# Kernel optimization log

Hardware: AMD Instinct MI355X
Metric: run time of the kernel (lower is better)

Reference implementation:

```python
import jax, jax.numpy as jnp
import numpy as np
import math

LOG_2PI = math.log(2.0 * math.pi)
ETA = 1.0        # Beta(gamma_1=1, gamma_2=eta) stick-breaking prior (gamma buffers at init)
MC_NUM = 4096    # Monte-Carlo samples
T_CLUSTER = 2    # trunc (must be 2: original normalize_factor broadcast requires it)
T_CLS = 2        # classifier DP truncation
DIM = 1024
N = 65536


def mix_weights(b):
    # stick-breaking: pad(b,(0,1),1) * pad(cumprod(1-b),(1,0),1); b: [..., T] -> [..., T+1]
    b1m = jnp.cumprod(1.0 - b, axis=-1)
    ones = jnp.ones((*b.shape[:-1], 1), b.dtype)
    return jnp.concatenate([b, ones], axis=-1) * jnp.concatenate([ones, b1m], axis=-1)


def gauss_log_prob(x, mu, rho):
    # diag Gaussian log-prob summed over feature dim; x [N,D], mu/rho [T,D] -> [N,T]
    std = jnp.log1p(jnp.exp(rho))                      # sigma = log(1+exp(rho))
    inv_var = 1.0 / (std * std)
    const = -0.5 * x.shape[-1] * LOG_2PI - jnp.sum(jnp.log(std), axis=-1)  # [T]
    # 0.5*sum((x-mu)^2/var) expanded as matmuls to avoid an [N,T,D] intermediate
    quad = 0.5 * ((x * x) @ inv_var.T) - x @ (mu * inv_var).T \
           + 0.5 * jnp.sum(mu * mu * inv_var, axis=-1)
    return const - quad


def gauss_entropy(rho):
    # mean over T of diag-Gaussian entropies; rho [T,D] -> scalar
    D = rho.shape[-1]
    std = jnp.log1p(jnp.exp(rho))
    ent = 0.5 * D * (LOG_2PI + 1.0) + jnp.sum(jnp.log(std), axis=-1)  # [T]
    return jnp.mean(ent)


def setup_inputs() -> dict:
    key = jax.random.key(0)
    ks = jax.random.split(key, 5)
    return {
        "x": jax.random.normal(ks[0], (N, DIM), jnp.float32),
        "mu_c": jax.random.normal(ks[1], (T_CLUSTER, DIM), jnp.float32),
        "rho_c": jax.random.normal(ks[2], (T_CLUSTER, DIM), jnp.float32),
        "mu_f": jax.random.normal(ks[3], (T_CLS, DIM), jnp.float32),
        "rho_f": jax.random.normal(ks[4], (T_CLS, DIM), jnp.float32),
    }


def reference(x, mu_c, rho_c, mu_f, rho_f):
    key = jax.random.key(1)
    k1, k2, k3, k4, k5 = jax.random.split(key, 5)

    # ---- D_P_cluster.likelihood(x) ----
    beta_lik = jax.random.beta(k1, 1.0, ETA, (x.shape[0], T_CLUSTER), x.dtype)
    pi_lik = mix_weights(beta_lik)[:, :-1]                 # [N, T]
    ent = gauss_entropy(rho_c)                             # scalar
    log_pdfs = gauss_log_prob(x, mu_c, rho_c)              # [N, T]
    phi = jax.nn.softmax(jnp.log(pi_lik) + ent + log_pdfs, axis=-1)
    neg_likelihood = -jnp.mean(jnp.sum(phi * (ent + log_pdfs), axis=1))

    # ---- MC sampling from the cluster mixture (fused, no Python loop) ----
    betas = jax.random.beta(k2, 1.0, ETA, (MC_NUM, T_CLUSTER), x.dtype)
    w = mix_weights(betas)[:, :-1]                         # [MC, T]
    w = w / jnp.sum(w, axis=1, keepdims=True)              # row-normalize (T==2 makes this exact)
    draws = jax.random.categorical(k3, jnp.log(w), axis=-1)  # [MC] component indices
    eps = jax.random.normal(k4, (MC_NUM, DIM), x.dtype)
    std_c = jnp.log1p(jnp.exp(rho_c))
    mc_samples = mu_c[draws] + std_c[draws] * eps          # [MC, D] reparametrized

    # ---- D_P_clssfy.infer(mc_samples) ----
    beta_inf = jax.random.beta(k5, 1.0, ETA, (MC_NUM, T_CLS), x.dtype)
    pi_inf = mix_weights(beta_inf)[:, :-1]                 # [MC, 2]
    lp_inf = gauss_log_prob(mc_samples, mu_f, rho_f)       # [MC, 2]
    logits = pi_inf * jax.nn.softmax(lp_inf, axis=1)
    return logits, neg_likelihood
```

## Files before the change

kernel.cpp:

```cpp
#include <hip/hip_runtime.h>
#include <hip/hip_bf16.h>
#include <stdint.h>

#define LOG2PI_F 1.8378770664093453f
#define D_DIM 1024
#define N_ROWS 65536
#define MC_ROWS 4096

__device__ __forceinline__ uint32_t mix64_32(uint64_t z) {
    z ^= z >> 33; z *= 0xff51afd7ed558ccdULL;
    z ^= z >> 33; z *= 0xc4ceb9fe1a85ec53ULL;
    z ^= z >> 33;
    return (uint32_t)z;
}
__device__ __forceinline__ float unif01(uint32_t stream, uint32_t idx) {
    uint32_t h = mix64_32(((uint64_t)stream << 32) | (uint64_t)idx);
    return (float)(h >> 9) * 0x1p-23f + 0x1p-24f;
}
__device__ __forceinline__ float softplusf(float r) { return log1pf(expf(r)); }

union F4 { float4 v; float f[4]; };

__global__ __launch_bounds__(256) void hdp_lik_kernel(
    const float* __restrict__ x, const float* __restrict__ mu_c,
    const float* __restrict__ rho_c, double* __restrict__ partial)
{
    __shared__ float H0[D_DIM], A0[D_DIM], H1[D_DIM], A1[D_DIM];
    __shared__ float red[1024];
    __shared__ float Vb[2];
    __shared__ double wpart[4];
    const int tid = threadIdx.x;

    float sls0 = 0.f, sls1 = 0.f, bq0 = 0.f, bq1 = 0.f;
    {
        const int d = tid * 4;
        F4 r0, r1, m0, m1;
        r0.v = *(const float4*)(rho_c + d);
        r1.v = *(const float4*)(rho_c + D_DIM + d);
        m0.v = *(const float4*)(mu_c + d);
        m1.v = *(const float4*)(mu_c + D_DIM + d);
#pragma unroll
        for (int e = 0; e < 4; ++e) {
            float s0 = softplusf(r0.f[e]);
            float i0 = 1.f / (s0 * s0);
            H0[d + e] = 0.5f * i0; A0[d + e] = m0.f[e] * i0;
            sls0 += logf(s0); bq0 += 0.5f * m0.f[e] * m0.f[e] * i0;
            float s1 = softplusf(r1.f[e]);
            float i1 = 1.f / (s1 * s1);
            H1[d + e] = 0.5f * i1; A1[d + e] = m1.f[e] * i1;
            sls1 += logf(s1); bq1 += 0.5f * m1.f[e] * m1.f[e] * i1;
        }
    }
    red[tid] = sls0; red[256 + tid] = sls1; red[512 + tid] = bq0; red[768 + tid] = bq1;
    __syncthreads();
    for (int s = 128; s > 0; s >>= 1) {
        if (tid < s) {
            red[tid]       += red[tid + s];
            red[256 + tid] += red[256 + tid + s];
            red[512 + tid] += red[512 + tid + s];
            red[768 + tid] += red[768 + tid + s];
        }
        __syncthreads();
    }
    if (tid == 0) {
        float SLS0 = red[0], SLS1 = red[256], BQ0 = red[512], BQ1 = red[768];
        float ent = 0.5f * 1024.f * (LOG2PI_F + 1.f) + 0.5f * (SLS0 + SLS1);
        Vb[0] = ent - 0.5f * 1024.f * LOG2PI_F - SLS0 - BQ0;
        Vb[1] = ent - 0.5f * 1024.f * LOG2PI_F - SLS1 - BQ1;
    }
    __syncthreads();

    const int wid = tid >> 6, lane = tid & 63;
    const float V0 = Vb[0], V1 = Vb[1];
    double wsum = 0.0;
    const int rowbase = blockIdx.x * 64 + wid * 16;
    for (int g = 0; g < 4; ++g) {
        const int r0 = rowbase + g * 4;
        float q0[4] = {0.f, 0.f, 0.f, 0.f}, q1[4] = {0.f, 0.f, 0.f, 0.f};
#pragma unroll
        for (int k = 0; k < 4; ++k) {
            const int d = k * 256 + lane * 4;
            F4 h0, a0v, h1, a1v;
            h0.v  = *(const float4*)&H0[d];
            a0v.v = *(const float4*)&A0[d];
            h1.v  = *(const float4*)&H1[d];
            a1v.v = *(const float4*)&A1[d];
#pragma unroll
            for (int r = 0; r < 4; ++r) {
                F4 xv; xv.v = *(const float4*)(x + (size_t)(r0 + r) * D_DIM + d);
#pragma unroll
                for (int e = 0; e < 4; ++e) {
                    float xe = xv.f[e];
                    float xx = xe * xe;
                    q0[r] = fmaf(xx, h0.f[e], q0[r]);  q0[r] = fmaf(-xe, a0v.f[e], q0[r]);
                    q1[r] = fmaf(xx, h1.f[e], q1[r]);  q1[r] = fmaf(-xe, a1v.f[e], q1[r]);
                }
            }
        }
#pragma unroll
        for (int r = 0; r < 4; ++r) {
            float a = q0[r], b = q1[r];
#pragma unroll
            for (int off = 32; off; off >>= 1) { a += __shfl_xor(a, off); b += __shfl_xor(b, off); }
            const uint32_t row = (uint32_t)(r0 + r);
            float u0 = unif01(1u, 2u * row), u1v = unif01(1u, 2u * row + 1u);
            float lp0 = logf(u0);
            float lp1 = logf(u1v) + logf(1.f - u0);
            float v0 = V0 - a, v1 = V1 - b;
            float s0 = lp0 + v0, s1 = lp1 + v1;
            float mx = fmaxf(s0, s1);
            float e0 = expf(s0 - mx), e1 = expf(s1 - mx);
            float phi0 = e0 / (e0 + e1);
            wsum += (double)(phi0 * v0 + (1.f - phi0) * v1);
        }
    }
    if (lane == 0) wpart[wid] = wsum;
    __syncthreads();
    if (tid == 0) partial[blockIdx.x] = wpart[0] + wpart[1] + wpart[2] + wpart[3];
}

__global__ __launch_bounds__(256) void hdp_cls_kernel(
    const float* __restrict__ mu_c, const float* __restrict__ rho_c,
    const float* __restrict__ mu_f, const float* __restrict__ rho_f,
    float* __restrict__ out)
{
    __shared__ float MU0[D_DIM], SD0[D_DIM], MU1[D_DIM], SD1[D_DIM];
    __shared__ float HF0[D_DIM], AF0[D_DIM], HF1[D_DIM], AF1[D_DIM];
    __shared__ float red[1024];
    __shared__ float CF[2];
    const int tid = threadIdx.x;

    float slsf0 = 0.f, slsf1 = 0.f, bqf0 = 0.f, bqf1 = 0.f;
    {
        const int d = tid * 4;
#pragma unroll
        for (int e = 0; e < 4; ++e) {
            MU0[d + e] = mu_c[d + e];           SD0[d + e] = softplusf(rho_c[d + e]);
            MU1[d + e] = mu_c[D_DIM + d + e];   SD1[d + e] = softplusf(rho_c[D_DIM + d + e]);
            float mf0 = mu_f[d + e], sf0 = softplusf(rho_f[d + e]);
            float i0 = 1.f / (sf0 * sf0);
            HF0[d + e] = 0.5f * i0; AF0[d + e] = mf0 * i0;
            slsf0 += logf(sf0); bqf0 += 0.5f * mf0 * mf0 * i0;
            float mf1 = mu_f[D_DIM + d + e], sf1 = softplusf(rho_f[D_DIM + d + e]);
            float i1 = 1.f / (sf1 * sf1);
            HF1[d + e] = 0.5f * i1; AF1[d + e] = mf1 * i1;
            slsf1 += logf(sf1); bqf1 += 0.5f * mf1 * mf1 * i1;
        }
    }
    red[tid] = slsf0; red[256 + tid] = slsf1; red[512 + tid] = bqf0; red[768 + tid] = bqf1;
    __syncthreads();
    for (int s = 128; s > 0; s >>= 1) {
        if (tid < s) {
            red[tid]       += red[tid + s];
            red[256 + tid] += red[256 + tid + s];
            red[512 + tid] += red[512 + tid + s];
            red[768 + tid] += red[768 + tid + s];
        }
        __syncthreads();
    }
    if (tid == 0) {
        CF[0] = -0.5f * 1024.f * LOG2PI_F - red[0]   - red[512];
        CF[1] = -0.5f * 1024.f * LOG2PI_F - red[256] - red[768];
    }
    __syncthreads();

    const int wid = tid >> 6, lane = tid & 63;
    const float CF0 = CF[0], CF1 = CF[1];
    for (int r = 0; r < 4; ++r) {
        const uint32_t j = (uint32_t)blockIdx.x * 16u + (uint32_t)wid * 4u + (uint32_t)r;
        float b0 = unif01(2u, 2u * j), b1 = unif01(2u, 2u * j + 1u);
        float wn0 = b0 / (b0 + b1 * (1.f - b0));
        int dr = (unif01(3u, j) < wn0) ? 0 : 1;
        float bi0 = unif01(5u, 2u * j), bi1 = unif01(5u, 2u * j + 1u);
        float pi0 = bi0, pi1 = bi1 * (1.f - bi0);
        const float* MU = dr ? &MU1[0] : &MU0[0];
        const float* SD = dr ? &SD1[0] : &SD0[0];
        float qf0 = 0.f, qf1 = 0.f;
#pragma unroll
        for (int k = 0; k < 4; ++k) {
            const int dd = k * 256 + lane * 4;
            F4 mu, sd, h0, a0, h1, a1;
            mu.v = *(const float4*)&MU[dd];
            sd.v = *(const float4*)&SD[dd];
            h0.v = *(const float4*)&HF0[dd];
            a0.v = *(const float4*)&AF0[dd];
            h1.v = *(const float4*)&HF1[dd];
            a1.v = *(const float4*)&AF1[dd];
#pragma unroll
            for (int e = 0; e < 4; e += 2) {
                uint32_t p = j * 512u + (uint32_t)((dd + e) >> 1);
                float uu1 = unif01(4u, p), uu2 = unif01(6u, p);
                float rad = sqrtf(-2.f * logf(uu1));
                float sn, cs;
                __sincosf(6.283185307179586f * uu2, &sn, &cs);
                float mc0 = fmaf(sd.f[e],     rad * cs, mu.f[e]);
                float mc1 = fmaf(sd.f[e + 1], rad * sn, mu.f[e + 1]);
                float xx0 = mc0 * mc0, xx1 = mc1 * mc1;
                qf0 = fmaf(xx0, h0.f[e], qf0);      qf0 = fmaf(-mc0, a0.f[e], qf0);
                qf0 = fmaf(xx1, h0.f[e + 1], qf0);  qf0 = fmaf(-mc1, a0.f[e + 1], qf0);
                qf1 = fmaf(xx0, h1.f[e], qf1);      qf1 = fmaf(-mc0, a1.f[e], qf1);
                qf1 = fmaf(xx1, h1.f[e + 1], qf1);  qf1 = fmaf(-mc1, a1.f[e + 1], qf1);
            }
        }
#pragma unroll
        for (int off = 32; off; off >>= 1) { qf0 += __shfl_xor(qf0, off); qf1 += __shfl_xor(qf1, off); }
        float lp0 = CF0 - qf0, lp1 = CF1 - qf1;
        float mx = fmaxf(lp0, lp1);
        float e0 = expf(lp0 - mx), e1 = expf(lp1 - mx);
        float inv = 1.f / (e0 + e1);
        if (lane == 0) {
            out[2u * j]      = pi0 * e0 * inv;
            out[2u * j + 1u] = pi1 * e1 * inv;
        }
    }
}

__global__ void hdp_final_kernel(const double* __restrict__ partial,
                                 float* __restrict__ out)
{
    const int lane = threadIdx.x;
    double s = 0.0;
    for (int i = lane; i < 1024; i += 64) s += partial[i];
#pragma unroll
    for (int off = 32; off; off >>= 1) s += __shfl_xor(s, off);
    if (lane == 0) out[8192] = (float)(-s / 65536.0);
}

extern "C" void kernel_launch(void* const* d_in, const int* in_sizes, int n_in,
                              void* d_out, int out_size, void* d_ws, size_t ws_size,
                              hipStream_t stream) {
    const float* x     = (const float*)d_in[0];
    const float* mu_c  = (const float*)d_in[1];
    const float* rho_c = (const float*)d_in[2];
    const float* mu_f  = (const float*)d_in[3];
    const float* rho_f = (const float*)d_in[4];
    float* out = (float*)d_out;
    double* partial = (double*)d_ws;

    hipLaunchKernelGGL(hdp_lik_kernel, dim3(1024), dim3(256), 0, stream,
                       x, mu_c, rho_c, partial);
    hipLaunchKernelGGL(hdp_cls_kernel, dim3(256), dim3(256), 0, stream,
                       mu_c, rho_c, mu_f, rho_f, out);
    hipLaunchKernelGGL(hdp_final_kernel, dim3(1), dim3(64), 0, stream,
                       partial, out);
}
```

Before: 70.35 us.

## Fuse likelihood and classifier kernels into one interleaved grid launch

Merges the likelihood and MC-classifier kernels into one launch of 2304 blocks, where every ninth block does classifier work and the other eight process 32 x-rows each. The grid now has 2048 likelihood blocks instead of 1024. The shared-memory tree reductions become wave shuffles plus a 4-entry combine, and x is read with nontemporal loads. The aim is to remove a kernel launch and overlap the compute-heavy classifier blocks with the bandwidth-bound x streaming. In exchange, softplus of rho_c is recomputed per element in classifier blocks, and the final reduction now sums 2048 partials.

```diff
diff --git a/kernel.cpp b/kernel.cpp
--- a/kernel.cpp
+++ b/kernel.cpp
@@ -1,11 +1,10 @@
 #include <hip/hip_runtime.h>
-#include <hip/hip_bf16.h>
 #include <stdint.h>
 
 #define LOG2PI_F 1.8378770664093453f
 #define D_DIM 1024
-#define N_ROWS 65536
-#define MC_ROWS 4096
+
+typedef float v4f __attribute__((ext_vector_type(4)));
 
 __device__ __forceinline__ uint32_t mix64_32(uint64_t z) {
     z ^= z >> 33; z *= 0xff51afd7ed558ccdULL;
@@ -19,26 +18,33 @@
 }
 __device__ __forceinline__ float softplusf(float r) { return log1pf(expf(r)); }
 
-union F4 { float4 v; float f[4]; };
-
-__global__ __launch_bounds__(256) void hdp_lik_kernel(
+union F4 { v4f v; float f[4]; };
+
+__global__ __launch_bounds__(256) void hdp_main_kernel(
     const float* __restrict__ x, const float* __restrict__ mu_c,
-    const float* __restrict__ rho_c, double* __restrict__ partial)
+    const float* __restrict__ rho_c, const float* __restrict__ mu_f,
+    const float* __restrict__ rho_f, float* __restrict__ out,
+    double* __restrict__ partial)
 {
     __shared__ float H0[D_DIM], A0[D_DIM], H1[D_DIM], A1[D_DIM];
-    __shared__ float red[1024];
-    __shared__ float Vb[2];
+    __shared__ float wred[4][4];
     __shared__ double wpart[4];
-    const int tid = threadIdx.x;
-
+
+    const int bid = blockIdx.x;
+    const int q = bid / 9, rr = bid % 9;
+    const bool is_cls = (rr == 4);
+    const int tid = threadIdx.x, wid = tid >> 6, lane = tid & 63;
+
+    const float* mu_s  = is_cls ? mu_f  : mu_c;
+    const float* rho_s = is_cls ? rho_f : rho_c;
     float sls0 = 0.f, sls1 = 0.f, bq0 = 0.f, bq1 = 0.f;
     {
         const int d = tid * 4;
         F4 r0, r1, m0, m1;
-        r0.v = *(const float4*)(rho_c + d);
-        r1.v = *(const float4*)(rho_c + D_DIM + d);
-        m0.v = *(const float4*)(mu_c + d);
-        m1.v = *(const float4*)(mu_c + D_DIM + d);
+        r0.v = *(const v4f*)(rho_s + d);
+        r1.v = *(const v4f*)(rho_s + D_DIM + d);
+        m0.v = *(const v4f*)(mu_s + d);
+        m1.v = *(const v4f*)(mu_s + D_DIM + d);
 #pragma unroll
         for (int e = 0; e < 4; ++e) {
             float s0 = softplusf(r0.f[e]);
@@ -51,179 +57,139 @@
             sls1 += logf(s1); bq1 += 0.5f * m1.f[e] * m1.f[e] * i1;
         }
     }
-    red[tid] = sls0; red[256 + tid] = sls1; red[512 + tid] = bq0; red[768 + tid] = bq1;
+#pragma unroll
+    for (int off = 32; off; off >>= 1) {
+        sls0 += __shfl_xor(sls0, off); sls1 += __shfl_xor(sls1, off);
+        bq0  += __shfl_xor(bq0,  off); bq1  += __shfl_xor(bq1,  off);
+    }
+    if (lane == 0) {
+        wred[wid][0] = sls0; wred[wid][1] = sls1;
+        wred[wid][2] = bq0;  wred[wid][3] = bq1;
+    }
     __syncthreads();
-    for (int s = 128; s > 0; s >>= 1) {
-        if (tid < s) {
-            red[tid]       += red[tid + s];
-            red[256 + tid] += red[256 + tid + s];
-            red[512 + tid] += red[512 + tid + s];
-            red[768 + tid] += red[768 + tid + s];
+    const float SLS0 = wred[0][0] + wred[1][0] + wred[2][0] + wred[3][0];
+    const float SLS1 = wred[0][1] + wred[1][1] + wred[2][1] + wred[3][1];
+    const float BQ0  = wred[0][2] + wred[1][2] + wred[2][2] + wred[3][2];
+    const float BQ1  = wred[0][3] + wred[1][3] + wred[2][3] + wred[3][3];
+    const float CF0 = -0.5f * 1024.f * LOG2PI_F - SLS0 - BQ0;
+    const float CF1 = -0.5f * 1024.f * LOG2PI_F - SLS1 - BQ1;
+
+    if (!is_cls) {
+        const float ent = 0.5f * 1024.f * (LOG2PI_F + 1.f) + 0.5f * (SLS0 + SLS1);
+        const float V0 = CF0 + ent, V1 = CF1 + ent;
+        const int lik_blk = q * 8 + (rr < 4 ? rr : rr - 1);
+        const int rowbase = lik_blk * 32 + wid * 8;
+        double wsum = 0.0;
+#pragma unroll
+        for (int g = 0; g < 2; ++g) {
+            const int r0 = rowbase + g * 4;
+            float q0[4] = {0.f, 0.f, 0.f, 0.f}, q1[4] = {0.f, 0.f, 0.f, 0.f};
+#pragma unroll
+            for (int k = 0; k < 4; ++k) {
+                const int d = k * 256 + lane * 4;
+                F4 h0, a0v, h1, a1v;
+                h0.v  = *(const v4f*)&H0[d];
+                a0v.v = *(const v4f*)&A0[d];
+                h1.v  = *(const v4f*)&H1[d];
+                a1v.v = *(const v4f*)&A1[d];
+#pragma unroll
+                for (int r = 0; r < 4; ++r) {
+                    F4 xv;
+                    xv.v = __builtin_nontemporal_load(
+                        (const v4f*)(x + (size_t)(r0 + r) * D_DIM + d));
+#pragma unroll
+                    for (int e = 0; e < 4; ++e) {
+                        float xe = xv.f[e];
+                        float xx = xe * xe;
+                        q0[r] = fmaf(xx, h0.f[e], q0[r]);  q0[r] = fmaf(-xe, a0v.f[e], q0[r]);
+                        q1[r] = fmaf(xx, h1.f[e], q1[r]);  q1[r] = fmaf(-xe, a1v.f[e], q1[r]);
+                    }
+                }
+            }
+#pragma unroll
+            for (int r = 0; r < 4; ++r) {
+                float a = q0[r], b = q1[r];
+#pragma unroll
+                for (int off = 32; off; off >>= 1) { a += __shfl_xor(a, off); b += __shfl_xor(b, off); }
+                const uint32_t row = (uint32_t)(r0 + r);
+                float u0 = unif01(1u, 2u * row), u1v = unif01(1u, 2u * row + 1u);
+                float lp0 = logf(u0);
+                float lp1 = logf(u1v) + logf(1.f - u0);
+                float v0 = V0 - a, v1 = V1 - b;
+                float s0 = lp0 + v0, s1 = lp1 + v1;
+                float mx = fmaxf(s0, s1);
+                float e0 = expf(s0 - mx), e1 = expf(s1 - mx);
+                float phi0 = e0 / (e0 + e1);
+                wsum += (double)(phi0 * v0 + (1.f - phi0) * v1);
+            }
         }
+        if (lane == 0) wpart[wid] = wsum;
         __syncthreads();
-    }
-    if (tid == 0) {
-        float SLS0 = red[0], SLS1 = red[256], BQ0 = red[512], BQ1 = red[768];
-        float ent = 0.5f * 1024.f * (LOG2PI_F + 1.f) + 0.5f * (SLS0 + SLS1);
-        Vb[0] = ent - 0.5f * 1024.f * LOG2PI_F - SLS0 - BQ0;
-        Vb[1] = ent - 0.5f * 1024.f * LOG2PI_F - SLS1 - BQ1;
-    }
+        if (tid == 0) partial[lik_blk] = wpart[0] + wpart[1] + wpart[2] + wpart[3];
+    } else {
+        for (int r = 0; r < 4; ++r) {
+            const uint32_t j = (uint32_t)q * 16u + (uint32_t)wid * 4u + (uint32_t)r;
+            float b0 = unif01(2u, 2u * j), b1 = unif01(2u, 2u * j + 1u);
+            float wn0 = b0 / (b0 + b1 * (1.f - b0));
+            int dr = (unif01(3u, j) < wn0) ? 0 : 1;
+            float bi0 = unif01(5u, 2u * j), bi1 = unif01(5u, 2u * j + 1u);
+            float pi0 = bi0, pi1 = bi1 * (1.f - bi0);
+            const float* MUg = mu_c + (size_t)dr * D_DIM;
+            const float* RHg = rho_c + (size_t)dr * D_DIM;
+            float qf0 = 0.f, qf1 = 0.f;
+#pragma unroll
+            for (int k = 0; k < 4; ++k) {
+                const int dd = k * 256 + lane * 4;
+                F4 mu, rh, h0, a0, h1, a1;
+                mu.v = *(const v4f*)(MUg + dd);
+                rh.v = *(const v4f*)(RHg + dd);
+                h0.v = *(const v4f*)&H0[dd];
+                a0.v = *(const v4f*)&A0[dd];
+                h1.v = *(const v4f*)&H1[dd];
+                a1.v = *(const v4f*)&A1[dd];
+#pragma unroll
+                for (int e = 0; e < 4; e += 2) {
+                    uint32_t p = j * 512u + (uint32_t)((dd + e) >> 1);
+                    float uu1 = unif01(4u, p), uu2 = unif01(6u, p);
+                    float rad = sqrtf(-2.f * logf(uu1));
+                    float sn, cs;
+                    __sincosf(6.283185307179586f * uu2, &sn, &cs);
+                    float sd0 = softplusf(rh.f[e]), sd1 = softplusf(rh.f[e + 1]);
+                    float mc0 = fmaf(sd0, rad * cs, mu.f[e]);
+                    float mc1 = fmaf(sd1, rad * sn, mu.f[e + 1]);
+                    float xx0 = mc0 * mc0, xx1 = mc1 * mc1;
+                    qf0 = fmaf(xx0, h0.f[e], qf0);      qf0 = fmaf(-mc0, a0.f[e], qf0);
+                    qf0 = fmaf(xx1, h0.f[e + 1], qf0);  qf0 = fmaf(-mc1, a0.f[e + 1], qf0);
+                    qf1 = fmaf(xx0, h1.f[e], qf1);      qf1 = fmaf(-mc0, a1.f[e], qf1);
+                    qf1 = fmaf(xx1, h1.f[e + 1], qf1);  qf1 = fmaf(-mc1, a1.f[e + 1], qf1);
+                }
+            }
+#pragma unroll
+            for (int off = 32; off; off >>= 1) { qf0 += __shfl_xor(qf0, off); qf1 += __shfl_xor(qf1, off); }
+            float lp0 = CF0 - qf0, lp1 = CF1 - qf1;
+            float mx = fmaxf(lp0, lp1);
+            float e0 = expf(lp0 - mx), e1 = expf(lp1 - mx);
+            float inv = 1.f / (e0 + e1);
+            if (lane == 0) {
+                out[2u * j]      = pi0 * e0 * inv;
+                out[2u * j + 1u] = pi1 * e1 * inv;
+            }
+        }
+    }
+}
+
+__global__ __launch_bounds__(256) void hdp_final_kernel(
+    const double* __restrict__ partial, float* __restrict__ out)
+{
+    __shared__ double wp[4];
+    const int tid = threadIdx.x, wid = tid >> 6, lane = tid & 63;
+    double s = 0.0;
+    for (int i = tid; i < 2048; i += 256) s += partial[i];
+#pragma unroll
+    for (int off = 32; off; off >>= 1) s += __shfl_xor(s, off);
+    if (lane == 0) wp[wid] = s;
     __syncthreads();
-
-    const int wid = tid >> 6, lane = tid & 63;
-    const float V0 = Vb[0], V1 = Vb[1];
-    double wsum = 0.0;
-    const int rowbase = blockIdx.x * 64 + wid * 16;
-    for (int g = 0; g < 4; ++g) {
-        const int r0 = rowbase + g * 4;
-        float q0[4] = {0.f, 0.f, 0.f, 0.f}, q1[4] = {0.f, 0.f, 0.f, 0.f};
-#pragma unroll
-        for (int k = 0; k < 4; ++k) {
-            const int d = k * 256 + lane * 4;
-            F4 h0, a0v, h1, a1v;
-            h0.v  = *(const float4*)&H0[d];
-            a0v.v = *(const float4*)&A0[d];
-            h1.v  = *(const float4*)&H1[d];
-            a1v.v = *(const float4*)&A1[d];
-#pragma unroll
-            for (int r = 0; r < 4; ++r) {
-                F4 xv; xv.v = *(const float4*)(x + (size_t)(r0 + r) * D_DIM + d);
-#pragma unroll
-                for (int e = 0; e < 4; ++e) {
-                    float xe = xv.f[e];
-                    float xx = xe * xe;
-                    q0[r] = fmaf(xx, h0.f[e], q0[r]);  q0[r] = fmaf(-xe, a0v.f[e], q0[r]);
-                    q1[r] = fmaf(xx, h1.f[e], q1[r]);  q1[r] = fmaf(-xe, a1v.f[e], q1[r]);
-                }
-            }
-        }
-#pragma unroll
-        for (int r = 0; r < 4; ++r) {
-            float a = q0[r], b = q1[r];
-#pragma unroll
-            for (int off = 32; off; off >>= 1) { a += __shfl_xor(a, off); b += __shfl_xor(b, off); }
-            const uint32_t row = (uint32_t)(r0 + r);
-            float u0 = unif01(1u, 2u * row), u1v = unif01(1u, 2u * row + 1u);
-            float lp0 = logf(u0);
-            float lp1 = logf(u1v) + logf(1.f - u0);
-            float v0 = V0 - a, v1 = V1 - b;
-            float s0 = lp0 + v0, s1 = lp1 + v1;
-            float mx = fmaxf(s0, s1);
-            float e0 = expf(s0 - mx), e1 = expf(s1 - mx);
-            float phi0 = e0 / (e0 + e1);
-            wsum += (double)(phi0 * v0 + (1.f - phi0) * v1);
-        }
-    }
-    if (lane == 0) wpart[wid] = wsum;
-    __syncthreads();
-    if (tid == 0) partial[blockIdx.x] = wpart[0] + wpart[1] + wpart[2] + wpart[3];
-}
-
-__global__ __launch_bounds__(256) void hdp_cls_kernel(
-    const float* __restrict__ mu_c, const float* __restrict__ rho_c,
-    const float* __restrict__ mu_f, const float* __restrict__ rho_f,
-    float* __restrict__ out)
-{
-    __shared__ float MU0[D_DIM], SD0[D_DIM], MU1[D_DIM], SD1[D_DIM];
-    __shared__ float HF0[D_DIM], AF0[D_DIM], HF1[D_DIM], AF1[D_DIM];
-    __shared__ float red[1024];
-    __shared__ float CF[2];
-    const int tid = threadIdx.x;
-
-    float slsf0 = 0.f, slsf1 = 0.f, bqf0 = 0.f, bqf1 = 0.f;
-    {
-        const int d = tid * 4;
-#pragma unroll
-        for (int e = 0; e < 4; ++e) {
-            MU0[d + e] = mu_c[d + e];           SD0[d + e] = softplusf(rho_c[d + e]);
-            MU1[d + e] = mu_c[D_DIM + d + e];   SD1[d + e] = softplusf(rho_c[D_DIM + d + e]);
-            float mf0 = mu_f[d + e], sf0 = softplusf(rho_f[d + e]);
-            float i0 = 1.f / (sf0 * sf0);
-            HF0[d + e] = 0.5f * i0; AF0[d + e] = mf0 * i0;
-            slsf0 += logf(sf0); bqf0 += 0.5f * mf0 * mf0 * i0;
-            float mf1 = mu_f[D_DIM + d + e], sf1 = softplusf(rho_f[D_DIM + d + e]);
-            float i1 = 1.f / (sf1 * sf1);
-            HF1[d + e] = 0.5f * i1; AF1[d + e] = mf1 * i1;
-            slsf1 += logf(sf1); bqf1 += 0.5f * mf1 * mf1 * i1;
-        }
-    }
-    red[tid] = slsf0; red[256 + tid] = slsf1; red[512 + tid] = bqf0; red[768 + tid] = bqf1;
-    __syncthreads();
-    for (int s = 128; s > 0; s >>= 1) {
-        if (tid < s) {
-            red[tid]       += red[tid + s];
-            red[256 + tid] += red[256 + tid + s];
-            red[512 + tid] += red[512 + tid + s];
-            red[768 + tid] += red[768 + tid + s];
-        }
-        __syncthreads();
-    }
-    if (tid == 0) {
-        CF[0] = -0.5f * 1024.f * LOG2PI_F - red[0]   - red[512];
-        CF[1] = -0.5f * 1024.f * LOG2PI_F - red[256] - red[768];
-    }
-    __syncthreads();
-
-    const int wid = tid >> 6, lane = tid & 63;
-    const float CF0 = CF[0], CF1 = CF[1];
-    for (int r = 0; r < 4; ++r) {
-        const uint32_t j = (uint32_t)blockIdx.x * 16u + (uint32_t)wid * 4u + (uint32_t)r;
-        float b0 = unif01(2u, 2u * j), b1 = unif01(2u, 2u * j + 1u);
-        float wn0 = b0 / (b0 + b1 * (1.f - b0));
-        int dr = (unif01(3u, j) < wn0) ? 0 : 1;
-        float bi0 = unif01(5u, 2u * j), bi1 = unif01(5u, 2u * j + 1u);
-        float pi0 = bi0, pi1 = bi1 * (1.f - bi0);
-        const float* MU = dr ? &MU1[0] : &MU0[0];
-        const float* SD = dr ? &SD1[0] : &SD0[0];
-        float qf0 = 0.f, qf1 = 0.f;
-#pragma unroll
-        for (int k = 0; k < 4; ++k) {
-            const int dd = k * 256 + lane * 4;
-            F4 mu, sd, h0, a0, h1, a1;
-            mu.v = *(const float4*)&MU[dd];
-            sd.v = *(const float4*)&SD[dd];
-            h0.v = *(const float4*)&HF0[dd];
-            a0.v = *(const float4*)&AF0[dd];
-            h1.v = *(const float4*)&HF1[dd];
-            a1.v = *(const float4*)&AF1[dd];
-#pragma unroll
-            for (int e = 0; e < 4; e += 2) {
-                uint32_t p = j * 512u + (uint32_t)((dd + e) >> 1);
-                float uu1 = unif01(4u, p), uu2 = unif01(6u, p);
-                float rad = sqrtf(-2.f * logf(uu1));
-                float sn, cs;
-                __sincosf(6.283185307179586f * uu2, &sn, &cs);
-                float mc0 = fmaf(sd.f[e],     rad * cs, mu.f[e]);
-                float mc1 = fmaf(sd.f[e + 1], rad * sn, mu.f[e + 1]);
-                float xx0 = mc0 * mc0, xx1 = mc1 * mc1;
-                qf0 = fmaf(xx0, h0.f[e], qf0);      qf0 = fmaf(-mc0, a0.f[e], qf0);
-                qf0 = fmaf(xx1, h0.f[e + 1], qf0);  qf0 = fmaf(-mc1, a0.f[e + 1], qf0);
-                qf1 = fmaf(xx0, h1.f[e], qf1);      qf1 = fmaf(-mc0, a1.f[e], qf1);
-                qf1 = fmaf(xx1, h1.f[e + 1], qf1);  qf1 = fmaf(-mc1, a1.f[e + 1], qf1);
-            }
-        }
-#pragma unroll
-        for (int off = 32; off; off >>= 1) { qf0 += __shfl_xor(qf0, off); qf1 += __shfl_xor(qf1, off); }
-        float lp0 = CF0 - qf0, lp1 = CF1 - qf1;
-        float mx = fmaxf(lp0, lp1);
-        float e0 = expf(lp0 - mx), e1 = expf(lp1 - mx);
-        float inv = 1.f / (e0 + e1);
-        if (lane == 0) {
-            out[2u * j]      = pi0 * e0 * inv;
-            out[2u * j + 1u] = pi1 * e1 * inv;
-        }
-    }
-}
-
-__global__ void hdp_final_kernel(const double* __restrict__ partial,
-                                 float* __restrict__ out)
-{
-    const int lane = threadIdx.x;
-    double s = 0.0;
-    for (int i = lane; i < 1024; i += 64) s += partial[i];
-#pragma unroll
-    for (int off = 32; off; off >>= 1) s += __shfl_xor(s, off);
-    if (lane == 0) out[8192] = (float)(-s / 65536.0);
+    if (tid == 0) out[8192] = (float)(-(wp[0] + wp[1] + wp[2] + wp[3]) / 65536.0);
 }
 
 extern "C" void kernel_launch(void* const* d_in, const int* in_sizes, int n_in,
@@ -237,10 +203,8 @@
     float* out = (float*)d_out;
     double* partial = (double*)d_ws;
 
-    hipLaunchKernelGGL(hdp_lik_kernel, dim3(1024), dim3(256), 0, stream,
-                       x, mu_c, rho_c, partial);
-    hipLaunchKernelGGL(hdp_cls_kernel, dim3(256), dim3(256), 0, stream,
-                       mu_c, rho_c, mu_f, rho_f, out);
-    hipLaunchKernelGGL(hdp_final_kernel, dim3(1), dim3(64), 0, stream,
+    hipLaunchKernelGGL(hdp_main_kernel, dim3(2304), dim3(256), 0, stream,
+                       x, mu_c, rho_c, mu_f, rho_f, out, partial);
+    hipLaunchKernelGGL(hdp_final_kernel, dim3(1), dim3(256), 0, stream,
                        partial, out);
 }
```

New measurement: 97.31 us. 1.38x slower.
